# Optimization experiments

Measured on AMD Instinct MI355X. Metric: run time of the kernel, lower is better.

The kernel has to match this reference:

```python
import jax, jax.numpy as jnp
import numpy as np

B, N, D = 8, 256, 64  # batch, n_entities, feature dim


def setup_inputs() -> dict:
    key = jax.random.key(0)
    ks = jax.random.split(key, 8)
    s = 0.02
    return {
        "emb1": jax.random.normal(ks[0], (B, N, D), jnp.float32),
        "emb2": jax.random.normal(ks[1], (B, N, N, D), jnp.float32),
        "W1a": jax.random.normal(ks[2], (3 * D, 128), jnp.float32) * s,
        "b1a": jnp.zeros((128,), jnp.float32),
        "W1b": jax.random.normal(ks[3], (128, D), jnp.float32) * s,
        "b1b": jnp.zeros((D,), jnp.float32),
        "W2a": jax.random.normal(ks[4], (4 * D, 256), jnp.float32) * s,
        "b2a": jnp.zeros((256,), jnp.float32),
        "W2b": jax.random.normal(ks[5], (256, D), jnp.float32) * s,
        "b2b": jnp.zeros((D,), jnp.float32),
    }


def _mlp(x, Wa, ba, Wb, bb):
    h = jax.nn.relu(jnp.einsum("...i,io->...o", x, Wa) + ba)
    return jnp.einsum("...i,io->...o", h, Wb) + bb


def reference(emb1, emb2, W1a, b1a, W1b, b1b, W2a, b2a, W2b, b2b):
    # arity 1: reduce arity-2 embedding over second entity dim (max & min), concat
    red_max = jnp.max(emb2, axis=-2)           # [B,N,D]
    red_min = jnp.min(emb2, axis=-2)           # [B,N,D]
    cat1 = jnp.concatenate([emb1, red_max, red_min], axis=-1)  # [B,N,3D]

    # arity 2: expand arity-1 embedding along a new entity dim, concat with emb2
    exp = jnp.broadcast_to(emb1[:, :, None, :], emb2.shape)    # [B,N,N,D]
    cat2 = jnp.concatenate([exp, emb2], axis=-1)               # [B,N,N,2D]

    # permutation gather: position (i,j) gets [cat2[j,i], cat2[i,j]] along features
    perm2 = jnp.concatenate([jnp.transpose(cat2, (0, 2, 1, 3)), cat2], axis=-1)  # [B,N,N,4D]

    out1 = _mlp(cat1, W1a, b1a, W1b, b1b)    # [B,N,D]
    out2 = _mlp(perm2, W2a, b2a, W2b, b2b)   # [B,N,N,D]
    return (out1, out2)
```

## Files before the change

kernel.cpp:

```cpp
#include <hip/hip_runtime.h>
#include <hip/hip_bf16.h>

typedef __bf16 bf16x8 __attribute__((ext_vector_type(8)));
typedef float f32x4 __attribute__((ext_vector_type(4)));
typedef unsigned int u32;
typedef unsigned short u16;
typedef u32 u32x4 __attribute__((ext_vector_type(4)));
typedef u16 u16x4 __attribute__((ext_vector_type(4)));
typedef u16 u16x8 __attribute__((ext_vector_type(8)));

__device__ __forceinline__ u16 f2bf(float x) {
  u32 u = __float_as_uint(x);
  return (u16)((u + 0x7FFFu + ((u >> 16) & 1u)) >> 16);
}
__device__ __forceinline__ u16 cvt_bf16(float x) {
  __bf16 h = (__bf16)x;
  return __builtin_bit_cast(u16, h);
}

__device__ __forceinline__ bf16x8 ld_frag_lds(const u16* base, int byteOff) {
  u32x4 v = *(const u32x4*)((const char*)base + byteOff);
  return __builtin_bit_cast(bf16x8, v);
}
__device__ __forceinline__ bf16x8 ld_frag_glb(const u16* p) {
  u32x4 v = *(const u32x4*)p;
  return __builtin_bit_cast(bf16x8, v);
}

__global__ void prep_w_kernel(const float* __restrict__ W2a, const float* __restrict__ W2b,
                              u16* __restrict__ wfA, u16* __restrict__ wfB2) {
  int t = blockIdx.x * 256 + threadIdx.x;
  if (t < 8192) {
    int lane = t & 63;
    int ks = (t >> 6) & 7;
    int ntg = t >> 9;
    int col = (ntg << 4) + (lane & 15);
    int kb = (ks << 5) + ((lane >> 4) << 3);
#pragma unroll
    for (int q = 0; q < 8; ++q)
      wfA[t * 8 + q] = f2bf(W2a[(kb + q) * 256 + col]);
  } else if (t < 10240) {
    int t2i = t - 8192;
    int lane = t2i & 63;
    int dt = (t2i >> 6) & 3;
    int tt = (t2i >> 8) & 1;
    int w = t2i >> 9;
    int g = lane >> 4, c = lane & 15;
    int col = (dt << 4) + c;
#pragma unroll
    for (int q = 0; q < 8; ++q) {
      int pi = (q < 4) ? (g * 4 + q) : (16 + g * 4 + (q - 4));
      int n = w * 64 + tt * 32 + pi;
      wfB2[t2i * 8 + q] = f2bf(W2b[n * 64 + col]);
    }
  }
}

__global__ __launch_bounds__(256) void out1_kernel(
    const float* __restrict__ emb1, const float* __restrict__ emb2,
    const float* __restrict__ W1a, const float* __restrict__ b1a,
    const float* __restrict__ W1b, const float* __restrict__ b1b,
    float* __restrict__ out1) {
  int bi = blockIdx.x;
  int t = threadIdx.x;
  __shared__ float smax[4][64];
  __shared__ float smin[4][64];
  __shared__ float cat1[192];
  __shared__ float h[128];

  int d = t & 63, q = t >> 6;
  const float* base = emb2 + (size_t)bi * 256 * 64;
  float vmax = -INFINITY, vmin = INFINITY;
  for (int j = q; j < 256; j += 4) {
    float v = base[j * 64 + d];
    vmax = fmaxf(vmax, v);
    vmin = fminf(vmin, v);
  }
  smax[q][d] = vmax;
  smin[q][d] = vmin;
  __syncthreads();
  if (t < 64) {
    float mx = fmaxf(fmaxf(smax[0][t], smax[1][t]), fmaxf(smax[2][t], smax[3][t]));
    float mn = fminf(fminf(smin[0][t], smin[1][t]), fminf(smin[2][t], smin[3][t]));
    cat1[t] = emb1[bi * 64 + t];
    cat1[64 + t] = mx;
    cat1[128 + t] = mn;
  }
  __syncthreads();
  if (t < 128) {
    float acc = b1a[t];
    for (int k = 0; k < 192; ++k) acc += cat1[k] * W1a[k * 128 + t];
    h[t] = fmaxf(acc, 0.f);
  }
  __syncthreads();
  if (t < 64) {
    float acc = b1b[t];
    for (int k = 0; k < 128; ++k) acc += h[k] * W1b[k * 64 + t];
    out1[bi * 64 + t] = acc;
  }
}

__global__ __launch_bounds__(256, 2) void out2_kernel(
    const float* __restrict__ emb1, const float* __restrict__ emb2,
    const float* __restrict__ b2a, const float* __restrict__ b2b,
    const u16* __restrict__ wfA, const u16* __restrict__ wfB2,
    float* __restrict__ out2) {
  __shared__ __align__(16) u16 SH[24576];

  int blk = blockIdx.x;
  int b = blk >> 10;
  int i = (blk >> 2) & 255;
  int j0 = (blk & 3) << 6;
  int t = threadIdx.x;
  int lane = t & 63;
  int w = t >> 6;
  int lr = lane & 15;
  int lg = lane >> 4;

  {
    int r = t >> 2;
    int c16 = (t & 3) << 4;
    const float* s0 = emb1 + ((b << 8) + j0 + r) * 64;
    const float* s1 = emb2 + ((((size_t)(b << 8) + j0 + r) << 8) + i) * 64;
    const float* s2 = emb1 + ((b << 8) + i) * 64;
    const float* s3 = emb2 + ((((size_t)(b << 8) + i) << 8) + (j0 + r)) * 64;
    const float* srcs[4] = {s0, s1, s2, s3};
#pragma unroll
    for (int seg = 0; seg < 4; ++seg) {
      const float* src = srcs[seg];
#pragma unroll
      for (int u = 0; u < 2; ++u) {
        int d = c16 + (u << 3);
        float4 v0 = *(const float4*)(src + d);
        float4 v1 = *(const float4*)(src + d + 4);
        u16x8 o = {cvt_bf16(v0.x), cvt_bf16(v0.y), cvt_bf16(v0.z), cvt_bf16(v0.w),
                   cvt_bf16(v1.x), cvt_bf16(v1.y), cvt_bf16(v1.z), cvt_bf16(v1.w)};
        int byteOff = (r * 512 + ((seg << 6) + d) * 2) ^ ((r & 7) << 4);
        *(u16x8*)((char*)SH + byteOff) = o;
      }
    }
  }
  __syncthreads();

  f32x4 acc1[4][4];
#pragma unroll
  for (int m = 0; m < 4; ++m)
#pragma unroll
    for (int nt = 0; nt < 4; ++nt) acc1[m][nt] = (f32x4){0.f, 0.f, 0.f, 0.f};

#pragma unroll
  for (int ks = 0; ks < 8; ++ks) {
    int kByte = (ks << 6) + (lg << 4);
    bf16x8 a[4];
#pragma unroll
    for (int m = 0; m < 4; ++m) {
      int row = (m << 4) + lr;
      a[m] = ld_frag_lds(SH, (row * 512 + kByte) ^ ((lr & 7) << 4));
    }
    bf16x8 bw[4];
#pragma unroll
    for (int nt = 0; nt < 4; ++nt)
      bw[nt] = ld_frag_glb(wfA + (size_t)((((w << 2) + nt) * 8 + ks) * 64 + lane) * 8);
#pragma unroll
    for (int m = 0; m < 4; ++m)
#pragma unroll
      for (int nt = 0; nt < 4; ++nt)
        acc1[m][nt] = __builtin_amdgcn_mfma_f32_16x16x32_bf16(bw[nt], a[m], acc1[m][nt], 0, 0, 0);
  }

  __syncthreads();

  f32x4 acc2[4][4];
#pragma unroll
  for (int m = 0; m < 4; ++m)
#pragma unroll
    for (int dt = 0; dt < 4; ++dt) acc2[m][dt] = (f32x4){0.f, 0.f, 0.f, 0.f};

#pragma unroll
  for (int t2 = 0; t2 < 2; ++t2) {
    int nbase = (w << 6) + (t2 << 5) + (lg << 2);
    float4 ba = *(const float4*)(b2a + nbase);
    float4 bb = *(const float4*)(b2a + nbase + 16);
    bf16x8 h[4];
#pragma unroll
    for (int m = 0; m < 4; ++m) {
      f32x4 pa = acc1[m][2 * t2];
      f32x4 pb = acc1[m][2 * t2 + 1];
      u16x8 hp = {cvt_bf16(fmaxf(pa[0] + ba.x, 0.f)), cvt_bf16(fmaxf(pa[1] + ba.y, 0.f)),
                  cvt_bf16(fmaxf(pa[2] + ba.z, 0.f)), cvt_bf16(fmaxf(pa[3] + ba.w, 0.f)),
                  cvt_bf16(fmaxf(pb[0] + bb.x, 0.f)), cvt_bf16(fmaxf(pb[1] + bb.y, 0.f)),
                  cvt_bf16(fmaxf(pb[2] + bb.z, 0.f)), cvt_bf16(fmaxf(pb[3] + bb.w, 0.f))};
      h[m] = __builtin_bit_cast(bf16x8, hp);
    }
#pragma unroll
    for (int dt = 0; dt < 4; ++dt) {
      bf16x8 wf = ld_frag_glb(wfB2 + (size_t)(((((w << 1) + t2) << 2) + dt) * 64 + lane) * 8);
#pragma unroll
      for (int m = 0; m < 4; ++m)
        acc2[m][dt] = __builtin_amdgcn_mfma_f32_16x16x32_bf16(wf, h[m], acc2[m][dt], 0, 0, 0);
    }
  }

  char* red = (char*)SH;
#pragma unroll
  for (int dt = 0; dt < 4; ++dt) {
    if (dt != w) {
      int s = dt - (dt > w ? 1 : 0);
#pragma unroll
      for (int m = 0; m < 4; ++m)
        *(f32x4*)(red + ((((w * 3 + s) << 2) + m) << 10) + (lane << 4)) = acc2[m][dt];
    }
  }
  __syncthreads();

  f32x4 accO[4];
#pragma unroll
  for (int m = 0; m < 4; ++m) {
    accO[m] = acc2[m][0];
#pragma unroll
    for (int dt = 1; dt < 4; ++dt)
      if (w == dt) accO[m] = acc2[m][dt];
  }
#pragma unroll
  for (int wp = 0; wp < 4; ++wp) {
    if (wp != w) {
      int s = w - (w > wp ? 1 : 0);
#pragma unroll
      for (int m = 0; m < 4; ++m) {
        f32x4 p = *(const f32x4*)(red + ((((wp * 3 + s) << 2) + m) << 10) + (lane << 4));
        accO[m] += p;
      }
    }
  }

  float4 bias2 = *(const float4*)(b2b + (w << 4) + (lg << 2));
  float* obase = out2 + (((size_t)(b << 8) + i) * 256 + j0) * 64 + (w << 4) + (lg << 2);
#pragma unroll
  for (int m = 0; m < 4; ++m) {
    float4 v = {accO[m][0] + bias2.x, accO[m][1] + bias2.y,
                accO[m][2] + bias2.z, accO[m][3] + bias2.w};
    *(float4*)(obase + (size_t)((m << 4) + lr) * 64) = v;
  }
}

extern "C" void kernel_launch(void* const* d_in, const int* in_sizes, int n_in,
                              void* d_out, int out_size, void* d_ws, size_t ws_size,
                              hipStream_t stream) {
  const float* emb1 = (const float*)d_in[0];
  const float* emb2 = (const float*)d_in[1];
  const float* W1a  = (const float*)d_in[2];
  const float* b1a  = (const float*)d_in[3];
  const float* W1b  = (const float*)d_in[4];
  const float* b1b  = (const float*)d_in[5];
  const float* W2a  = (const float*)d_in[6];
  const float* b2a  = (const float*)d_in[7];
  const float* W2b  = (const float*)d_in[8];
  const float* b2b  = (const float*)d_in[9];

  float* out = (float*)d_out;
  u16* wfA  = (u16*)d_ws;
  u16* wfB2 = wfA + 65536;

  prep_w_kernel<<<40, 256, 0, stream>>>(W2a, W2b, wfA, wfB2);
  out1_kernel<<<2048, 256, 0, stream>>>(emb1, emb2, W1a, b1a, W1b, b1b, out);
  out2_kernel<<<8192, 256, 0, stream>>>(emb1, emb2, b2a, b2b, wfA, wfB2,
                                        out + 8 * 256 * 64);
}
```

Baseline: 152.6 us.

## Precompute emb1 projections of first MLP layer and fuse out1 into out2 launch

The broadcast emb1 segments of the arity-2 first-layer input are factored out. Their products with W2a are computed once per (b,n) in a new prep_T kernel (T0 folded into accumulator init, T2 plus bias folded into the ReLU bias), which halves the MFMA K dimension and the LDS staging in the main kernel. The out1 computation becomes extra blocks of the same launch, removing a separate kernel. The cost is an extra small kernel plus reading fp32 T0/T2 tiles from global memory per block.

```diff
diff --git a/kernel.cpp b/kernel.cpp
--- a/kernel.cpp
+++ b/kernel.cpp
@@ -30,17 +30,18 @@
 __global__ void prep_w_kernel(const float* __restrict__ W2a, const float* __restrict__ W2b,
                               u16* __restrict__ wfA, u16* __restrict__ wfB2) {
   int t = blockIdx.x * 256 + threadIdx.x;
-  if (t < 8192) {
+  if (t < 4096) {
     int lane = t & 63;
-    int ks = (t >> 6) & 7;
-    int ntg = t >> 9;
+    int ks = (t >> 6) & 3;
+    int ntg = t >> 8;
     int col = (ntg << 4) + (lane & 15);
-    int kb = (ks << 5) + ((lane >> 4) << 3);
+    int kk = (ks << 5) + ((lane >> 4) << 3);
+    int row = (kk < 64) ? (64 + kk) : (128 + kk);
 #pragma unroll
     for (int q = 0; q < 8; ++q)
-      wfA[t * 8 + q] = f2bf(W2a[(kb + q) * 256 + col]);
-  } else if (t < 10240) {
-    int t2i = t - 8192;
+      wfA[t * 8 + q] = f2bf(W2a[(row + q) * 256 + col]);
+  } else if (t < 6144) {
+    int t2i = t - 4096;
     int lane = t2i & 63;
     int dt = (t2i >> 6) & 3;
     int tt = (t2i >> 8) & 1;
@@ -56,111 +57,142 @@
   }
 }
 
-__global__ __launch_bounds__(256) void out1_kernel(
+__global__ __launch_bounds__(256) void prep_T_kernel(
+    const float* __restrict__ emb1, const float* __restrict__ W2a,
+    const float* __restrict__ b2a, float* __restrict__ T0p, float* __restrict__ T2p) {
+  __shared__ float e1row[64];
+  int bn = blockIdx.x;
+  int t = threadIdx.x;
+  if (t < 64) e1row[t] = emb1[bn * 64 + t];
+  __syncthreads();
+  float a0 = 0.f;
+  float a2 = b2a[t];
+#pragma unroll 8
+  for (int k = 0; k < 64; ++k) {
+    float e = e1row[k];
+    a0 += e * W2a[k * 256 + t];
+    a2 += e * W2a[(128 + k) * 256 + t];
+  }
+  T0p[(size_t)bn * 256 + t] = a0;
+  T2p[(size_t)bn * 256 + t] = a2;
+}
+
+__global__ __launch_bounds__(256, 2) void fused_kernel(
     const float* __restrict__ emb1, const float* __restrict__ emb2,
     const float* __restrict__ W1a, const float* __restrict__ b1a,
     const float* __restrict__ W1b, const float* __restrict__ b1b,
-    float* __restrict__ out1) {
-  int bi = blockIdx.x;
+    const float* __restrict__ b2b,
+    const u16* __restrict__ wfA, const u16* __restrict__ wfB2,
+    const float* __restrict__ T0p, const float* __restrict__ T2p,
+    float* __restrict__ out1, float* __restrict__ out2) {
+  __shared__ __align__(16) u16 SH[24576];
+
+  int blk = blockIdx.x;
   int t = threadIdx.x;
-  __shared__ float smax[4][64];
-  __shared__ float smin[4][64];
-  __shared__ float cat1[192];
-  __shared__ float h[128];
-
-  int d = t & 63, q = t >> 6;
-  const float* base = emb2 + (size_t)bi * 256 * 64;
-  float vmax = -INFINITY, vmin = INFINITY;
-  for (int j = q; j < 256; j += 4) {
-    float v = base[j * 64 + d];
-    vmax = fmaxf(vmax, v);
-    vmin = fminf(vmin, v);
-  }
-  smax[q][d] = vmax;
-  smin[q][d] = vmin;
-  __syncthreads();
-  if (t < 64) {
-    float mx = fmaxf(fmaxf(smax[0][t], smax[1][t]), fmaxf(smax[2][t], smax[3][t]));
-    float mn = fminf(fminf(smin[0][t], smin[1][t]), fminf(smin[2][t], smin[3][t]));
-    cat1[t] = emb1[bi * 64 + t];
-    cat1[64 + t] = mx;
-    cat1[128 + t] = mn;
-  }
-  __syncthreads();
-  if (t < 128) {
-    float acc = b1a[t];
-    for (int k = 0; k < 192; ++k) acc += cat1[k] * W1a[k * 128 + t];
-    h[t] = fmaxf(acc, 0.f);
-  }
-  __syncthreads();
-  if (t < 64) {
-    float acc = b1b[t];
-    for (int k = 0; k < 128; ++k) acc += h[k] * W1b[k * 64 + t];
-    out1[bi * 64 + t] = acc;
-  }
-}
-
-__global__ __launch_bounds__(256, 2) void out2_kernel(
-    const float* __restrict__ emb1, const float* __restrict__ emb2,
-    const float* __restrict__ b2a, const float* __restrict__ b2b,
-    const u16* __restrict__ wfA, const u16* __restrict__ wfB2,
-    float* __restrict__ out2) {
-  __shared__ __align__(16) u16 SH[24576];
-
-  int blk = blockIdx.x;
+
+  if (blk >= 8192) {
+    int bi = blk - 8192;
+    float* f = (float*)SH;
+    float* smax = f;
+    float* smin = f + 256;
+    float* cat1 = f + 512;
+    float* h    = f + 704;
+
+    int d = t & 63, q = t >> 6;
+    const float* base = emb2 + (size_t)bi * 256 * 64;
+    float vmax = -INFINITY, vmin = INFINITY;
+    for (int j = q; j < 256; j += 4) {
+      float v = base[j * 64 + d];
+      vmax = fmaxf(vmax, v);
+      vmin = fminf(vmin, v);
+    }
+    smax[q * 64 + d] = vmax;
+    smin[q * 64 + d] = vmin;
+    __syncthreads();
+    if (t < 64) {
+      float mx = fmaxf(fmaxf(smax[t], smax[64 + t]), fmaxf(smax[128 + t], smax[192 + t]));
+      float mn = fminf(fminf(smin[t], smin[64 + t]), fminf(smin[128 + t], smin[192 + t]));
+      cat1[t] = emb1[bi * 64 + t];
+      cat1[64 + t] = mx;
+      cat1[128 + t] = mn;
+    }
+    __syncthreads();
+    if (t < 128) {
+      float acc = b1a[t];
+      for (int k = 0; k < 192; ++k) acc += cat1[k] * W1a[k * 128 + t];
+      h[t] = fmaxf(acc, 0.f);
+    }
+    __syncthreads();
+    if (t < 64) {
+      float acc = b1b[t];
+      for (int k = 0; k < 128; ++k) acc += h[k] * W1b[k * 64 + t];
+      out1[bi * 64 + t] = acc;
+    }
+    return;
+  }
+
   int b = blk >> 10;
   int i = (blk >> 2) & 255;
   int j0 = (blk & 3) << 6;
-  int t = threadIdx.x;
   int lane = t & 63;
   int w = t >> 6;
   int lr = lane & 15;
   int lg = lane >> 4;
 
+  f32x4 acc1[4][4];
+  {
+    const float* T0b = T0p + ((size_t)(b << 8) + j0) * 256 + (w << 6) + (lg << 2);
+#pragma unroll
+    for (int m = 0; m < 4; ++m)
+#pragma unroll
+      for (int nt = 0; nt < 4; ++nt)
+        acc1[m][nt] = *(const f32x4*)(T0b + ((m << 4) + lr) * 256 + (nt << 4));
+  }
+  float4 t2v[4];
+  {
+    const float* T2b = T2p + ((size_t)(b << 8) + i) * 256 + (w << 6) + (lg << 2);
+#pragma unroll
+    for (int nt = 0; nt < 4; ++nt) t2v[nt] = *(const float4*)(T2b + (nt << 4));
+  }
+
   {
     int r = t >> 2;
-    int c16 = (t & 3) << 4;
-    const float* s0 = emb1 + ((b << 8) + j0 + r) * 64;
+    int q = t & 3;
     const float* s1 = emb2 + ((((size_t)(b << 8) + j0 + r) << 8) + i) * 64;
-    const float* s2 = emb1 + ((b << 8) + i) * 64;
-    const float* s3 = emb2 + ((((size_t)(b << 8) + i) << 8) + (j0 + r)) * 64;
-    const float* srcs[4] = {s0, s1, s2, s3};
-#pragma unroll
-    for (int seg = 0; seg < 4; ++seg) {
-      const float* src = srcs[seg];
-#pragma unroll
-      for (int u = 0; u < 2; ++u) {
-        int d = c16 + (u << 3);
-        float4 v0 = *(const float4*)(src + d);
-        float4 v1 = *(const float4*)(src + d + 4);
-        u16x8 o = {cvt_bf16(v0.x), cvt_bf16(v0.y), cvt_bf16(v0.z), cvt_bf16(v0.w),
-                   cvt_bf16(v1.x), cvt_bf16(v1.y), cvt_bf16(v1.z), cvt_bf16(v1.w)};
-        int byteOff = (r * 512 + ((seg << 6) + d) * 2) ^ ((r & 7) << 4);
-        *(u16x8*)((char*)SH + byteOff) = o;
-      }
+    const float* s2 = emb2 + ((((size_t)(b << 8) + i) << 8) + (j0 + r)) * 64;
+    const float* src = (q < 2) ? (s1 + (q << 5)) : (s2 + ((q - 2) << 5));
+    int swz = (r & 7) << 4;
+#pragma unroll
+    for (int c = 0; c < 2; ++c) {
+      const float* p = src + (c << 4);
+      float4 a0 = *(const float4*)(p);
+      float4 a1 = *(const float4*)(p + 4);
+      float4 a2 = *(const float4*)(p + 8);
+      float4 a3 = *(const float4*)(p + 12);
+      u16x8 o0 = {cvt_bf16(a0.x), cvt_bf16(a0.y), cvt_bf16(a0.z), cvt_bf16(a0.w),
+                  cvt_bf16(a1.x), cvt_bf16(a1.y), cvt_bf16(a1.z), cvt_bf16(a1.w)};
+      u16x8 o1 = {cvt_bf16(a2.x), cvt_bf16(a2.y), cvt_bf16(a2.z), cvt_bf16(a2.w),
+                  cvt_bf16(a3.x), cvt_bf16(a3.y), cvt_bf16(a3.z), cvt_bf16(a3.w)};
+      int base = r * 256 + (q << 6) + (c << 5);
+      *(u16x8*)((char*)SH + (base ^ swz)) = o0;
+      *(u16x8*)((char*)SH + ((base + 16) ^ swz)) = o1;
     }
   }
   __syncthreads();
 
-  f32x4 acc1[4][4];
-#pragma unroll
-  for (int m = 0; m < 4; ++m)
-#pragma unroll
-    for (int nt = 0; nt < 4; ++nt) acc1[m][nt] = (f32x4){0.f, 0.f, 0.f, 0.f};
-
-#pragma unroll
-  for (int ks = 0; ks < 8; ++ks) {
+#pragma unroll
+  for (int ks = 0; ks < 4; ++ks) {
     int kByte = (ks << 6) + (lg << 4);
     bf16x8 a[4];
 #pragma unroll
     for (int m = 0; m < 4; ++m) {
       int row = (m << 4) + lr;
-      a[m] = ld_frag_lds(SH, (row * 512 + kByte) ^ ((lr & 7) << 4));
+      a[m] = ld_frag_lds(SH, (row * 256 + kByte) ^ ((lr & 7) << 4));
     }
     bf16x8 bw[4];
 #pragma unroll
     for (int nt = 0; nt < 4; ++nt)
-      bw[nt] = ld_frag_glb(wfA + (size_t)((((w << 2) + nt) * 8 + ks) * 64 + lane) * 8);
+      bw[nt] = ld_frag_glb(wfA + (size_t)((((w << 2) + nt) * 4 + ks) * 64 + lane) * 8);
 #pragma unroll
     for (int m = 0; m < 4; ++m)
 #pragma unroll
@@ -178,9 +210,8 @@
 
 #pragma unroll
   for (int t2 = 0; t2 < 2; ++t2) {
-    int nbase = (w << 6) + (t2 << 5) + (lg << 2);
-    float4 ba = *(const float4*)(b2a + nbase);
-    float4 bb = *(const float4*)(b2a + nbase + 16);
+    float4 ba = t2v[2 * t2];
+    float4 bb = t2v[2 * t2 + 1];
     bf16x8 h[4];
 #pragma unroll
     for (int m = 0; m < 4; ++m) {
@@ -259,10 +290,13 @@
 
   float* out = (float*)d_out;
   u16* wfA  = (u16*)d_ws;
-  u16* wfB2 = wfA + 65536;
-
-  prep_w_kernel<<<40, 256, 0, stream>>>(W2a, W2b, wfA, wfB2);
-  out1_kernel<<<2048, 256, 0, stream>>>(emb1, emb2, W1a, b1a, W1b, b1b, out);
-  out2_kernel<<<8192, 256, 0, stream>>>(emb1, emb2, b2a, b2b, wfA, wfB2,
-                                        out + 8 * 256 * 64);
-}
+  u16* wfB2 = wfA + 32768;
+  float* T0p = (float*)(wfB2 + 16384);
+  float* T2p = T0p + 2048 * 256;
+
+  prep_w_kernel<<<24, 256, 0, stream>>>(W2a, W2b, wfA, wfB2);
+  prep_T_kernel<<<2048, 256, 0, stream>>>(emb1, W2a, b2a, T0p, T2p);
+  fused_kernel<<<10240, 256, 0, stream>>>(emb1, emb2, W1a, b1a, W1b, b1b,
+                                          b2b, wfA, wfB2, T0p, T2p,
+                                          out, out + 8 * 256 * 64);
+}
```

New measurement: 227.6 us. +49.2%, slower.
